# Kernel tuning notes

Hardware: AMD Instinct MI355X
Metric: run time of the kernel (lower is better)

The kernel has to match this reference:

```python
import jax, jax.numpy as jnp
import numpy as np

WIN = 5
EPS = 1e-05


def box_sum(x, win=WIN):
    """3D box-filter window sum, SAME padding (pad=win//2), via separable 1D convs.
    Mathematically identical to F.conv3d(x, ones(1,1,win,win,win), padding=win//2).
    x: [N, C, D, H, W]
    """
    pad = win // 2
    for ax in range(3):  # D, H, W
        kshape = [1, 1, 1, 1, 1]
        kshape[2 + ax] = win
        k = jnp.ones(kshape, x.dtype)
        pads = [(0, 0), (0, 0), (0, 0)]
        pads[ax] = (pad, pad)
        x = jax.lax.conv_general_dilated(
            x, k, window_strides=(1, 1, 1), padding=pads,
            dimension_numbers=('NCDHW', 'OIDHW', 'NCDHW'))
    return x


def setup_inputs() -> dict:
    key = jax.random.key(0)
    k1, k2 = jax.random.split(key)
    shape = (2, 1, 160, 192, 192)
    I = jax.random.normal(k1, shape, dtype=jnp.float32)
    J = jax.random.normal(k2, shape, dtype=jnp.float32)
    return {"I": I, "J": J}


def reference(I, J):
    V = float(WIN ** 3)  # window voxel count
    I_sum = box_sum(I)
    J_sum = box_sum(J)
    I2_sum = box_sum(I * I)
    J2_sum = box_sum(J * J)
    IJ_sum = box_sum(I * J)

    u_I = I_sum / V
    u_J = J_sum / V
    cross = IJ_sum - u_J * I_sum - u_I * J_sum + u_I * u_J * V
    I_var = I2_sum - 2.0 * u_I * I_sum + u_I * u_I * V
    J_var = J2_sum - 2.0 * u_J * J_sum + u_J * u_J * V
    cc = cross * cross / (I_var * J_var + EPS)
    # single channel: avg over channels is identity; loss = -mean(cc)
    return -1.0 * jnp.mean(cc)
```

## Files before the change

### kernel.cpp

```cpp
#include <hip/hip_runtime.h>


namespace {
constexpr int Wd = 192, Hd = 192, Dd = 160;
constexpr int SH = 192;
constexpr int SD = 192 * 192;
constexpr long SN = (long)SD * Dd;
constexpr int CD = 16;
constexpr int NCHUNK = 10;
constexpr int TROW = 68;
constexpr int ROWS = 20;
constexpr int SEGA = 17 * ROWS;
constexpr int TILEF = 2 * ROWS * TROW;
constexpr float INV_V = 1.0f / 125.0f;
constexpr float EPSf = 1e-5f;

__device__ __forceinline__ void wslide(const float h[8], float o[4]) {
  float s0 = h[0] + h[1] + h[2] + h[3] + h[4];
  float s1 = s0 - h[0] + h[5];
  float s2 = s1 - h[1] + h[6];
  float s3 = s2 - h[2] + h[7];
  o[0] = s0; o[1] = s1; o[2] = s2; o[3] = s3;
}

__device__ __forceinline__ void gl_lds16(const float* g, float* l) {
  __builtin_amdgcn_global_load_lds(
      (const __attribute__((address_space(1))) void*)g,
      (__attribute__((address_space(3))) void*)l, 16, 0, 0);
}
}

__global__ __launch_bounds__(256) void ncc_fused(const float* __restrict__ I,
                                                 const float* __restrict__ Jv,
                                                 float* __restrict__ out) {
  __shared__ float tile[2][TILEF];
  __shared__ float red[4];

  const int tid = threadIdx.x;
  const int tx = tid & 15;
  const int ty = tid >> 4;
  const int wbase = blockIdx.x * 64;
  const int hbase = blockIdx.y * 16;
  const int n  = blockIdx.z / NCHUNK;
  const int d_lo = (blockIdx.z % NCHUNK) * CD;

  const float* Ib = I  + (long)n * SN;
  const float* Jb = Jv + (long)n * SN;

  const int wave = tid >> 6, lane = tid & 63;
  const float* gsrc = (wave >= 2) ? Jb : Ib;
  int goff[3]; int loff[3]; bool on[3];
  #pragma unroll
  for (int r = 0; r < 3; ++r) {
    const int seg = wave * 170 + r * 64 + lane;
    on[r] = (r < 2) || (lane < 42);
    const int rem = seg % SEGA;
    const int row = rem / 17, c16 = rem % 17;
    const int hh = hbase + row - 2;
    const int hc = min(max(hh, 0), Hd - 1);
    const int gw = wbase - 2 + c16 * 4;
    const int gc = min(max(gw, 0), Wd - 4);
    goff[r] = hc * SH + gc;
    loff[r] = seg * 4;
  }

  {
    const int s0 = d_lo - 2;
    if (s0 >= 0 && s0 < Dd) {
      const float* base = gsrc + (long)s0 * SD;
      #pragma unroll
      for (int r = 0; r < 3; ++r) if (on[r]) gl_lds16(base + goff[r], &tile[0][loff[r]]);
    }
  }
  __syncthreads();

  const bool zl = (wbase == 0)   && (tx == 0);
  const bool zr = (wbase == 128) && (tx == 15);
  const bool hint = (hbase != 0) && (hbase != 176);

  float ring[5][5][4];
  float Dsum[5][4];
  #pragma unroll
  for (int c = 0; c < 5; ++c)
    #pragma unroll
    for (int k = 0; k < 4; ++k) {
      Dsum[c][k] = 0.f;
      #pragma unroll
      for (int q = 0; q < 5; ++q) ring[q][c][k] = 0.f;
    }
  float acc = 0.0f;

  constexpr int T = CD + 4;
  for (int t0 = 0; t0 < T; t0 += 5) {
    #pragma unroll
    for (int p = 0; p < 5; ++p) {
      const int t = t0 + p;
      const int s = d_lo - 2 + t;

      {
        const int sn = s + 1;
        if ((t + 1) < T && sn >= 0 && sn < Dd) {
          const float* base = gsrc + (long)sn * SD;
          float* dst = &tile[(t + 1) & 1][0];
          #pragma unroll
          for (int r = 0; r < 3; ++r) if (on[r]) gl_lds16(base + goff[r], dst + loff[r]);
        }
      }

      float hsI[8], hsJ[8], hsII[8], hsJJ[8], hsIJ[8];
      const bool svalid = (s >= 0) && (s < Dd);
      if (svalid && hint) {
        const float* bufc = &tile[t & 1][0];
        #pragma unroll
        for (int dh = 0; dh < 5; ++dh) {
          const float* pa = bufc + (ty + dh) * TROW + 4 * tx;
          const float* pb = pa + ROWS * TROW;
          float a[8], b[8];
          ((float4*)a)[0] = ((const float4*)pa)[0];
          ((float4*)a)[1] = ((const float4*)pa)[1];
          ((float4*)b)[0] = ((const float4*)pb)[0];
          ((float4*)b)[1] = ((const float4*)pb)[1];
          if (zl) { a[2]=a[0]; a[3]=a[1]; a[0]=0.f; a[1]=0.f;
                    b[2]=b[0]; b[3]=b[1]; b[0]=0.f; b[1]=0.f; }
          if (zr) { a[4]=a[6]; a[5]=a[7]; a[6]=0.f; a[7]=0.f;
                    b[4]=b[6]; b[5]=b[7]; b[6]=0.f; b[7]=0.f; }
          #pragma unroll
          for (int c = 0; c < 8; ++c) {
            const float x = a[c], y = b[c];
            if (dh == 0) {
              hsI[c] = x; hsJ[c] = y;
              hsII[c] = x * x; hsJJ[c] = y * y; hsIJ[c] = x * y;
            } else {
              hsI[c]  += x;
              hsJ[c]  += y;
              hsII[c] = fmaf(x, x, hsII[c]);
              hsJJ[c] = fmaf(y, y, hsJJ[c]);
              hsIJ[c] = fmaf(x, y, hsIJ[c]);
            }
          }
        }
      } else {
        #pragma unroll
        for (int c = 0; c < 8; ++c) {
          hsI[c] = 0.f; hsJ[c] = 0.f; hsII[c] = 0.f; hsJJ[c] = 0.f; hsIJ[c] = 0.f;
        }
        if (svalid) {
          const float* bufc = &tile[t & 1][0];
          #pragma unroll
          for (int dh = 0; dh < 5; ++dh) {
            const int hh = hbase + ty + dh - 2;
            if (hh >= 0 && hh < Hd) {
              const float* pa = bufc + (ty + dh) * TROW + 4 * tx;
              const float* pb = pa + ROWS * TROW;
              float a[8], b[8];
              ((float4*)a)[0] = ((const float4*)pa)[0];
              ((float4*)a)[1] = ((const float4*)pa)[1];
              ((float4*)b)[0] = ((const float4*)pb)[0];
              ((float4*)b)[1] = ((const float4*)pb)[1];
              if (zl) { a[2]=a[0]; a[3]=a[1]; a[0]=0.f; a[1]=0.f;
                        b[2]=b[0]; b[3]=b[1]; b[0]=0.f; b[1]=0.f; }
              if (zr) { a[4]=a[6]; a[5]=a[7]; a[6]=0.f; a[7]=0.f;
                        b[4]=b[6]; b[5]=b[7]; b[6]=0.f; b[7]=0.f; }
              #pragma unroll
              for (int c = 0; c < 8; ++c) {
                const float x = a[c], y = b[c];
                hsI[c]  += x;
                hsJ[c]  += y;
                hsII[c] = fmaf(x, x, hsII[c]);
                hsJJ[c] = fmaf(y, y, hsJJ[c]);
                hsIJ[c] = fmaf(x, y, hsIJ[c]);
              }
            }
          }
        }
      }

      float nw[5][4];
      wslide(hsI,  nw[0]);
      wslide(hsJ,  nw[1]);
      wslide(hsII, nw[2]);
      wslide(hsJJ, nw[3]);
      wslide(hsIJ, nw[4]);
      #pragma unroll
      for (int c = 0; c < 5; ++c)
        #pragma unroll
        for (int k = 0; k < 4; ++k) {
          Dsum[c][k] += nw[c][k] - ring[p][c][k];
          ring[p][c][k] = nw[c][k];
        }

      if (t >= 4) {
        #pragma unroll
        for (int k = 0; k < 4; ++k) {
          const float SI = Dsum[0][k], SJ = Dsum[1][k];
          const float SII = Dsum[2][k], SJJ = Dsum[3][k], SIJ = Dsum[4][k];
          const float cross = SIJ - SI * SJ * INV_V;
          const float vI    = SII - SI * SI * INV_V;
          const float vJ    = SJJ - SJ * SJ * INV_V;
          acc += cross * cross / (vI * vJ + EPSf);
        }
      }

      __syncthreads();
    }
  }

  #pragma unroll
  for (int off = 32; off > 0; off >>= 1) acc += __shfl_xor(acc, off, 64);
  if ((tid & 63) == 0) red[tid >> 6] = acc;
  __syncthreads();
  if (tid == 0) {
    const float total = red[0] + red[1] + red[2] + red[3];
    atomicAdd(out, total * (-1.0f / 11796480.0f));
  }
}

extern "C" void kernel_launch(void* const* d_in, const int* in_sizes, int n_in,
                              void* d_out, int out_size, void* d_ws, size_t ws_size,
                              hipStream_t stream) {
  const float* I = (const float*)d_in[0];
  const float* J = (const float*)d_in[1];
  float* out = (float*)d_out;
  hipMemsetAsync(out, 0, sizeof(float), stream);
  dim3 grid(3, 12, 2 * NCHUNK);
  ncc_fused<<<grid, 256, 0, stream>>>(I, J, out);
}
```

Before: 183.1 us.

## Triple-buffer LDS planes with partial vmcnt waits and split depth into smaller chunks

Replaces the double-buffered plane pipeline with a three-slot LDS ring. Each plane is prefetched two steps ahead, and the full barrier drain becomes an s_waitcnt vmcnt(3) plus s_barrier, so the next load can stay in flight while the current plane is computed. The depth chunk shrinks from 16 to 6 planes and the chunk count rises to 27, with a guard for the overhanging planes. This gives many more blocks for occupancy and latency hiding, at the cost of more halo plane reloads per output and a larger LDS footprint per block.

```diff
diff --git a/kernel.cpp b/kernel.cpp
--- a/kernel.cpp
+++ b/kernel.cpp
@@ -6,8 +6,8 @@
 constexpr int SH = 192;
 constexpr int SD = 192 * 192;
 constexpr long SN = (long)SD * Dd;
-constexpr int CD = 16;
-constexpr int NCHUNK = 10;
+constexpr int CD = 6;
+constexpr int NCHUNK = 27;
 constexpr int TROW = 68;
 constexpr int ROWS = 20;
 constexpr int SEGA = 17 * ROWS;
@@ -15,6 +15,9 @@
 constexpr float INV_V = 1.0f / 125.0f;
 constexpr float EPSf = 1e-5f;
 
+constexpr int WAITCNT_VM3 = 0x0F73;
+constexpr int WAITCNT_VM0 = 0x0F70;
+
 __device__ __forceinline__ void wslide(const float h[8], float o[4]) {
   float s0 = h[0] + h[1] + h[2] + h[3] + h[4];
   float s1 = s0 - h[0] + h[5];
@@ -33,7 +36,7 @@
 __global__ __launch_bounds__(256) void ncc_fused(const float* __restrict__ I,
                                                  const float* __restrict__ Jv,
                                                  float* __restrict__ out) {
-  __shared__ float tile[2][TILEF];
+  __shared__ __align__(16) float tile[3][TILEF];
   __shared__ float red[4];
 
   const int tid = threadIdx.x;
@@ -65,14 +68,20 @@
   }
 
   {
-    const int s0 = d_lo - 2;
+    const int s0 = d_lo - 2, s1 = d_lo - 1;
     if (s0 >= 0 && s0 < Dd) {
       const float* base = gsrc + (long)s0 * SD;
       #pragma unroll
       for (int r = 0; r < 3; ++r) if (on[r]) gl_lds16(base + goff[r], &tile[0][loff[r]]);
     }
-  }
-  __syncthreads();
+    if (s1 >= 0 && s1 < Dd) {
+      const float* base = gsrc + (long)s1 * SD;
+      #pragma unroll
+      for (int r = 0; r < 3; ++r) if (on[r]) gl_lds16(base + goff[r], &tile[1][loff[r]]);
+    }
+  }
+  __builtin_amdgcn_s_waitcnt(WAITCNT_VM0);
+  __builtin_amdgcn_s_barrier();
 
   const bool zl = (wbase == 0)   && (tx == 0);
   const bool zr = (wbase == 128) && (tx == 15);
@@ -91,46 +100,76 @@
   float acc = 0.0f;
 
   constexpr int T = CD + 4;
-  for (int t0 = 0; t0 < T; t0 += 5) {
-    #pragma unroll
-    for (int p = 0; p < 5; ++p) {
-      const int t = t0 + p;
-      const int s = d_lo - 2 + t;
-
-      {
-        const int sn = s + 1;
-        if ((t + 1) < T && sn >= 0 && sn < Dd) {
-          const float* base = gsrc + (long)sn * SD;
-          float* dst = &tile[(t + 1) & 1][0];
-          #pragma unroll
-          for (int r = 0; r < 3; ++r) if (on[r]) gl_lds16(base + goff[r], dst + loff[r]);
+  #pragma unroll
+  for (int t = 0; t < T; ++t) {
+    const int p = t % 5;
+    const int s = d_lo - 2 + t;
+
+    const bool issued = ((t + 2) < T) && ((d_lo + t) < Dd);
+    if (issued) {
+      const float* base = gsrc + (long)(d_lo + t) * SD;
+      float* dst = &tile[(t + 2) % 3][0];
+      #pragma unroll
+      for (int r = 0; r < 3; ++r) if (on[r]) gl_lds16(base + goff[r], dst + loff[r]);
+    }
+
+    float hsI[8], hsJ[8], hsII[8], hsJJ[8], hsIJ[8];
+    const bool svalid = (s >= 0) && (s < Dd);
+    if (svalid && hint) {
+      const float* bufc = &tile[t % 3][0];
+      #pragma unroll
+      for (int dh = 0; dh < 5; ++dh) {
+        const float* pa = bufc + (ty + dh) * TROW + 4 * tx;
+        const float* pb = pa + ROWS * TROW;
+        float a[8], b[8];
+        ((float4*)a)[0] = ((const float4*)pa)[0];
+        ((float4*)a)[1] = ((const float4*)pa)[1];
+        ((float4*)b)[0] = ((const float4*)pb)[0];
+        ((float4*)b)[1] = ((const float4*)pb)[1];
+        if (zl) { a[2]=a[0]; a[3]=a[1]; a[0]=0.f; a[1]=0.f;
+                  b[2]=b[0]; b[3]=b[1]; b[0]=0.f; b[1]=0.f; }
+        if (zr) { a[4]=a[6]; a[5]=a[7]; a[6]=0.f; a[7]=0.f;
+                  b[4]=b[6]; b[5]=b[7]; b[6]=0.f; b[7]=0.f; }
+        #pragma unroll
+        for (int c = 0; c < 8; ++c) {
+          const float x = a[c], y = b[c];
+          if (dh == 0) {
+            hsI[c] = x; hsJ[c] = y;
+            hsII[c] = x * x; hsJJ[c] = y * y; hsIJ[c] = x * y;
+          } else {
+            hsI[c]  += x;
+            hsJ[c]  += y;
+            hsII[c] = fmaf(x, x, hsII[c]);
+            hsJJ[c] = fmaf(y, y, hsJJ[c]);
+            hsIJ[c] = fmaf(x, y, hsIJ[c]);
+          }
         }
       }
-
-      float hsI[8], hsJ[8], hsII[8], hsJJ[8], hsIJ[8];
-      const bool svalid = (s >= 0) && (s < Dd);
-      if (svalid && hint) {
-        const float* bufc = &tile[t & 1][0];
+    } else {
+      #pragma unroll
+      for (int c = 0; c < 8; ++c) {
+        hsI[c] = 0.f; hsJ[c] = 0.f; hsII[c] = 0.f; hsJJ[c] = 0.f; hsIJ[c] = 0.f;
+      }
+      if (svalid) {
+        const float* bufc = &tile[t % 3][0];
         #pragma unroll
         for (int dh = 0; dh < 5; ++dh) {
-          const float* pa = bufc + (ty + dh) * TROW + 4 * tx;
-          const float* pb = pa + ROWS * TROW;
-          float a[8], b[8];
-          ((float4*)a)[0] = ((const float4*)pa)[0];
-          ((float4*)a)[1] = ((const float4*)pa)[1];
-          ((float4*)b)[0] = ((const float4*)pb)[0];
-          ((float4*)b)[1] = ((const float4*)pb)[1];
-          if (zl) { a[2]=a[0]; a[3]=a[1]; a[0]=0.f; a[1]=0.f;
-                    b[2]=b[0]; b[3]=b[1]; b[0]=0.f; b[1]=0.f; }
-          if (zr) { a[4]=a[6]; a[5]=a[7]; a[6]=0.f; a[7]=0.f;
-                    b[4]=b[6]; b[5]=b[7]; b[6]=0.f; b[7]=0.f; }
-          #pragma unroll
-          for (int c = 0; c < 8; ++c) {
-            const float x = a[c], y = b[c];
-            if (dh == 0) {
-              hsI[c] = x; hsJ[c] = y;
-              hsII[c] = x * x; hsJJ[c] = y * y; hsIJ[c] = x * y;
-            } else {
+          const int hh = hbase + ty + dh - 2;
+          if (hh >= 0 && hh < Hd) {
+            const float* pa = bufc + (ty + dh) * TROW + 4 * tx;
+            const float* pb = pa + ROWS * TROW;
+            float a[8], b[8];
+            ((float4*)a)[0] = ((const float4*)pa)[0];
+            ((float4*)a)[1] = ((const float4*)pa)[1];
+            ((float4*)b)[0] = ((const float4*)pb)[0];
+            ((float4*)b)[1] = ((const float4*)pb)[1];
+            if (zl) { a[2]=a[0]; a[3]=a[1]; a[0]=0.f; a[1]=0.f;
+                      b[2]=b[0]; b[3]=b[1]; b[0]=0.f; b[1]=0.f; }
+            if (zr) { a[4]=a[6]; a[5]=a[7]; a[6]=0.f; a[7]=0.f;
+                      b[4]=b[6]; b[5]=b[7]; b[6]=0.f; b[7]=0.f; }
+            #pragma unroll
+            for (int c = 0; c < 8; ++c) {
+              const float x = a[c], y = b[c];
               hsI[c]  += x;
               hsJ[c]  += y;
               hsII[c] = fmaf(x, x, hsII[c]);
@@ -139,70 +178,39 @@
             }
           }
         }
-      } else {
-        #pragma unroll
-        for (int c = 0; c < 8; ++c) {
-          hsI[c] = 0.f; hsJ[c] = 0.f; hsII[c] = 0.f; hsJJ[c] = 0.f; hsIJ[c] = 0.f;
-        }
-        if (svalid) {
-          const float* bufc = &tile[t & 1][0];
-          #pragma unroll
-          for (int dh = 0; dh < 5; ++dh) {
-            const int hh = hbase + ty + dh - 2;
-            if (hh >= 0 && hh < Hd) {
-              const float* pa = bufc + (ty + dh) * TROW + 4 * tx;
-              const float* pb = pa + ROWS * TROW;
-              float a[8], b[8];
-              ((float4*)a)[0] = ((const float4*)pa)[0];
-              ((float4*)a)[1] = ((const float4*)pa)[1];
-              ((float4*)b)[0] = ((const float4*)pb)[0];
-              ((float4*)b)[1] = ((const float4*)pb)[1];
-              if (zl) { a[2]=a[0]; a[3]=a[1]; a[0]=0.f; a[1]=0.f;
-                        b[2]=b[0]; b[3]=b[1]; b[0]=0.f; b[1]=0.f; }
-              if (zr) { a[4]=a[6]; a[5]=a[7]; a[6]=0.f; a[7]=0.f;
-                        b[4]=b[6]; b[5]=b[7]; b[6]=0.f; b[7]=0.f; }
-              #pragma unroll
-              for (int c = 0; c < 8; ++c) {
-                const float x = a[c], y = b[c];
-                hsI[c]  += x;
-                hsJ[c]  += y;
-                hsII[c] = fmaf(x, x, hsII[c]);
-                hsJJ[c] = fmaf(y, y, hsJJ[c]);
-                hsIJ[c] = fmaf(x, y, hsIJ[c]);
-              }
-            }
-          }
-        }
-      }
-
-      float nw[5][4];
-      wslide(hsI,  nw[0]);
-      wslide(hsJ,  nw[1]);
-      wslide(hsII, nw[2]);
-      wslide(hsJJ, nw[3]);
-      wslide(hsIJ, nw[4]);
-      #pragma unroll
-      for (int c = 0; c < 5; ++c)
-        #pragma unroll
-        for (int k = 0; k < 4; ++k) {
-          Dsum[c][k] += nw[c][k] - ring[p][c][k];
-          ring[p][c][k] = nw[c][k];
-        }
-
-      if (t >= 4) {
-        #pragma unroll
-        for (int k = 0; k < 4; ++k) {
-          const float SI = Dsum[0][k], SJ = Dsum[1][k];
-          const float SII = Dsum[2][k], SJJ = Dsum[3][k], SIJ = Dsum[4][k];
-          const float cross = SIJ - SI * SJ * INV_V;
-          const float vI    = SII - SI * SI * INV_V;
-          const float vJ    = SJJ - SJ * SJ * INV_V;
-          acc += cross * cross / (vI * vJ + EPSf);
-        }
-      }
-
-      __syncthreads();
-    }
+      }
+    }
+
+    float nw[5][4];
+    wslide(hsI,  nw[0]);
+    wslide(hsJ,  nw[1]);
+    wslide(hsII, nw[2]);
+    wslide(hsJJ, nw[3]);
+    wslide(hsIJ, nw[4]);
+    #pragma unroll
+    for (int c = 0; c < 5; ++c)
+      #pragma unroll
+      for (int k = 0; k < 4; ++k) {
+        Dsum[c][k] += nw[c][k] - ring[p][c][k];
+        ring[p][c][k] = nw[c][k];
+      }
+
+    const int d = d_lo + t - 4;
+    if (t >= 4 && d < Dd) {
+      #pragma unroll
+      for (int k = 0; k < 4; ++k) {
+        const float SI = Dsum[0][k], SJ = Dsum[1][k];
+        const float SII = Dsum[2][k], SJJ = Dsum[3][k], SIJ = Dsum[4][k];
+        const float cross = SIJ - SI * SJ * INV_V;
+        const float vI    = SII - SI * SI * INV_V;
+        const float vJ    = SJJ - SJ * SJ * INV_V;
+        acc += cross * cross / (vI * vJ + EPSf);
+      }
+    }
+
+    if (issued) __builtin_amdgcn_s_waitcnt(WAITCNT_VM3);
+    else        __builtin_amdgcn_s_waitcnt(WAITCNT_VM0);
+    __builtin_amdgcn_s_barrier();
   }
 
   #pragma unroll
```

Result: slower. 202.4 us (+10.5%).
